# Performance work log

Measured on AMD Instinct MI355X. Metric: run time of the kernel, lower is better.

Reference implementation:

```python
import jax, jax.numpy as jnp
import numpy as np

N_NODES = 200000
N_EVENTS = 200000
MEM_DIM = 128
MSG_DIM = 128
TIME_DIM = 16
MSG_IN = 2 * MEM_DIM + MSG_DIM + TIME_DIM  # 400


def setup_inputs() -> dict:
    key = jax.random.key(0)
    ks = jax.random.split(key, 12)
    return {
        "src_ids": jax.random.randint(ks[0], (N_EVENTS,), 0, N_NODES, dtype=jnp.int32),
        "dst_ids": jax.random.randint(ks[1], (N_EVENTS,), 0, N_NODES, dtype=jnp.int32),
        "edge_feat": jax.random.normal(ks[2], (N_EVENTS, MSG_DIM), dtype=jnp.float32),
        "timestamps": jax.random.uniform(ks[3], (N_EVENTS,), dtype=jnp.float32),
        "memory": jax.random.normal(ks[4], (N_NODES, MEM_DIM), dtype=jnp.float32) * 0.1,
        "last_update_time": jnp.zeros((N_NODES,), dtype=jnp.float32),
        "time_w": jax.random.normal(ks[5], (TIME_DIM,), dtype=jnp.float32),
        "time_phi": jnp.zeros((TIME_DIM,), dtype=jnp.float32),
        "W1": jax.random.normal(ks[6], (MSG_IN, MSG_DIM), dtype=jnp.float32) / np.sqrt(MSG_IN),
        "b1": jnp.zeros((MSG_DIM,), dtype=jnp.float32),
        "W2": jax.random.normal(ks[7], (MSG_DIM, MSG_DIM), dtype=jnp.float32) / np.sqrt(MSG_DIM),
        "b2": jnp.zeros((MSG_DIM,), dtype=jnp.float32),
        "W_ih": jax.random.normal(ks[8], (3 * MEM_DIM, MSG_DIM), dtype=jnp.float32) / np.sqrt(MSG_DIM),
        "W_hh": jax.random.normal(ks[9], (3 * MEM_DIM, MEM_DIM), dtype=jnp.float32) / np.sqrt(MEM_DIM),
        "b_ih": jnp.zeros((3 * MEM_DIM,), dtype=jnp.float32),
        "b_hh": jnp.zeros((3 * MEM_DIM,), dtype=jnp.float32),
    }


def _time_encode(dt, w, phi):
    # Time2Vec: linear first channel, sin on the rest
    wt = dt[:, None] * w[None, :] + phi[None, :]  # [E, TIME_DIM]
    return jnp.concatenate([wt[:, :1], jnp.sin(wt[:, 1:])], axis=-1)


def _message_mlp(x, W1, b1, W2, b2):
    h = jax.nn.relu(x @ W1 + b1)
    return h @ W2 + b2


def _gru_cell(x, h, W_ih, W_hh, b_ih, b_hh):
    gi = x @ W_ih.T + b_ih  # [U, 3H]
    gh = h @ W_hh.T + b_hh
    i_r, i_z, i_n = jnp.split(gi, 3, axis=-1)
    h_r, h_z, h_n = jnp.split(gh, 3, axis=-1)
    r = jax.nn.sigmoid(i_r + h_r)
    z = jax.nn.sigmoid(i_z + h_z)
    n = jnp.tanh(i_n + r * h_n)
    return (1.0 - z) * n + z * h


def reference(src_ids, dst_ids, edge_feat, timestamps, memory, last_update_time,
              time_w, time_phi, W1, b1, W2, b2, W_ih, W_hh, b_ih, b_hh):
    # 1) gather + time encode
    dt_src = timestamps - last_update_time[src_ids]
    dt_dst = timestamps - last_update_time[dst_ids]
    te_src = _time_encode(dt_src, time_w, time_phi)
    te_dst = _time_encode(dt_dst, time_w, time_phi)
    src_mem = memory[src_ids]
    dst_mem = memory[dst_ids]

    # 2) messages
    msg_src = _message_mlp(jnp.concatenate([src_mem, dst_mem, edge_feat, te_src], -1), W1, b1, W2, b2)
    msg_dst = _message_mlp(jnp.concatenate([dst_mem, src_mem, edge_feat, te_dst], -1), W1, b1, W2, b2)

    all_nodes = jnp.concatenate([src_ids, dst_ids])  # [2E]
    all_msgs = jnp.concatenate([msg_src, msg_dst], axis=0)  # [2E, MSG_DIM]

    # 3) 'last' aggregation: segment-max of positions, then gather
    pos = jnp.arange(all_nodes.shape[0], dtype=jnp.int32)
    last_pos = jax.ops.segment_max(pos, all_nodes, num_segments=N_NODES)  # int32 min where absent
    present = last_pos >= 0  # [N]
    agg = all_msgs[jnp.clip(last_pos, 0, None)]  # [N, MSG_DIM]
    agg = jnp.where(present[:, None], agg, 0.0)

    # 4) GRU memory update on involved nodes only
    new_mem = _gru_cell(agg, memory, W_ih, W_hh, b_ih, b_hh)
    memory_out = jnp.where(present[:, None], new_mem, memory)
    return memory_out
```

## Files before the change

### kernel.cpp

```cpp
#include <hip/hip_runtime.h>
#include <hip/hip_bf16.h>
#include <math.h>

#define NN 200000
#define NE 200000

typedef __attribute__((ext_vector_type(8))) short bf16x8;
typedef __attribute__((ext_vector_type(4))) float f32x4;

#define XASTR 136
#define XBSTR 296
#define OSTR  132
#define NT    (NN / 32)
#define PBT   (32 * XBSTR)

__device__ __forceinline__ float sigm(float x) { return 1.0f / (1.0f + __expf(-x)); }
__device__ __forceinline__ float tanh_f(float x) {
    float e = __expf(2.0f * x);
    return 1.0f - 2.0f / (e + 1.0f);
}
__device__ __forceinline__ ushort f2b(float x) {
    union { __hip_bfloat16 b; ushort u; } v;
    v.b = __float2bfloat16(x);
    return v.u;
}
__device__ __forceinline__ float b2f(ushort u) {
    return __uint_as_float(((unsigned)u) << 16);
}
__device__ __forceinline__ ushort4 cvt4(float4 v) {
    ushort4 u; u.x = f2b(v.x); u.y = f2b(v.y); u.z = f2b(v.z); u.w = f2b(v.w);
    return u;
}
__device__ __forceinline__ void gload_lds16(const ushort* g, ushort* l) {
    __builtin_amdgcn_global_load_lds(
        (const __attribute__((address_space(1))) unsigned int*)g,
        (__attribute__((address_space(3))) unsigned int*)l, 16, 0, 0);
}

#define MFMA16(a, b, c) __builtin_amdgcn_mfma_f32_16x16x32_bf16((a), (b), (c), 0, 0, 0)

#define NB_PREP 594
#define NB_SCAT (((2 * NE) + 255) / 256)
__global__ void k_pre(const float* __restrict__ W1, const float* __restrict__ W2,
                      const float* __restrict__ Wih, const float* __restrict__ Whh,
                      const float* __restrict__ b2, const float* __restrict__ bih,
                      ushort* __restrict__ W1F, ushort* __restrict__ W2IF,
                      ushort* __restrict__ WHF, float* __restrict__ cb,
                      const int* __restrict__ src, const int* __restrict__ dst,
                      int* __restrict__ last_pos) {
    int b = blockIdx.x;
    if (b >= NB_PREP) {
        int i = (b - NB_PREP) * 256 + threadIdx.x;
        if (i < NE) {
            atomicMax(&last_pos[src[i]], i);
        } else if (i < 2 * NE) {
            atomicMax(&last_pos[dst[i - NE]], i);
        }
        return;
    }
    int t = b * 256 + threadIdx.x;
    if (t < 104 * 512) {
        int f = t >> 9, idx = t & 511;
        int lane = idx >> 3, j = idx & 7, c16 = lane & 15, k8 = lane >> 4;
        int wvv = f / 26, r = f % 26, kt = r >> 1, ns = r & 1;
        int col = wvv * 32 + ns * 16 + c16;
        int kk = kt * 32 + k8 * 8 + j;
        W1F[t] = (kk < 400) ? f2b(W1[kk * 128 + col]) : (ushort)0;
        return;
    }
    t -= 104 * 512;
    if (t < 96 * 512) {
        int f = t >> 9, idx = t & 511;
        int lane = idx >> 3, j = idx & 7, c16 = lane & 15, k8 = lane >> 4;
        int wvv = f / 24, r = f % 24, kt = r / 6, rem = r % 6, g = rem >> 1, ns = rem & 1;
        int col = g * 128 + wvv * 32 + ns * 16 + c16;
        int kk = kt * 32 + k8 * 8 + j;
        float s = 0.0f;
        for (int c = 0; c < 128; ++c) s = fmaf(W2[kk * 128 + c], Wih[col * 128 + c], s);
        W2IF[f * 512 + idx] = f2b(s);
        return;
    }
    t -= 96 * 512;
    if (t < 96 * 512) {
        int f = t >> 9, idx = t & 511;
        int lane = idx >> 3, j = idx & 7, c16 = lane & 15, k8 = lane >> 4;
        int wvv = f / 24, r = f % 24, kt = r / 6, rem = r % 6, g = rem >> 1, ns = rem & 1;
        int col = g * 128 + wvv * 32 + ns * 16 + c16;
        int kk = kt * 32 + k8 * 8 + j;
        WHF[f * 512 + idx] = f2b(Whh[col * 128 + kk]);
        return;
    }
    t -= 96 * 512;
    if (t < 384) {
        float s = bih[t];
        for (int k = 0; k < 128; ++k) s = fmaf(b2[k], Wih[t * 128 + k], s);
        cb[t] = s;
    }
}

__global__ __launch_bounds__(256)
void k_gath(const int* __restrict__ last_pos,
            const int* __restrict__ src, const int* __restrict__ dst,
            const float* __restrict__ ts, const float* __restrict__ lut,
            const float* __restrict__ mem, const float* __restrict__ ef,
            const float* __restrict__ tw, const float* __restrict__ tphi,
            ushort* __restrict__ PB)
{
    const int wv = threadIdx.x >> 6, lane = threadIdx.x & 63;
    const int n0 = (blockIdx.x * 4 + wv) * 2;
    const int n1 = n0 + 1;
    const int l = lane & 31;
    const bool lo = lane < 32;

    const int p0 = last_pos[n0];
    const int p1 = last_pos[n1];

    float4 m0, f0, m1, f1;
    float te0 = 0.0f, te1 = 0.0f;
    if (p0 >= 0) {
        int e = (p0 < NE) ? p0 : p0 - NE;
        int o = (p0 < NE) ? dst[e] : src[e];
        if (lo) {
            m0 = *(const float4*)&mem[(size_t)o * 128 + l * 4];
            if (l < 16) {
                float dt = ts[e] - lut[n0];
                float w = fmaf(dt, tw[l], tphi[l]);
                te0 = (l == 0) ? w : __sinf(w);
            }
        } else {
            f0 = *(const float4*)&ef[(size_t)e * 128 + l * 4];
        }
    }
    if (p1 >= 0) {
        int e = (p1 < NE) ? p1 : p1 - NE;
        int o = (p1 < NE) ? dst[e] : src[e];
        if (lo) {
            m1 = *(const float4*)&mem[(size_t)o * 128 + l * 4];
            if (l < 16) {
                float dt = ts[e] - lut[n1];
                float w = fmaf(dt, tw[l], tphi[l]);
                te1 = (l == 0) ? w : __sinf(w);
            }
        } else {
            f1 = *(const float4*)&ef[(size_t)e * 128 + l * 4];
        }
    }

    if (p0 >= 0) {
        ushort* xb = PB + (size_t)n0 * XBSTR;
        if (lo) {
            *(ushort4*)&xb[l * 4] = cvt4(m0);
            xb[256 + l] = (l < 16) ? f2b(te0) : (ushort)0;
        } else {
            *(ushort4*)&xb[128 + l * 4] = cvt4(f0);
        }
    }
    if (p1 >= 0) {
        ushort* xb = PB + (size_t)n1 * XBSTR;
        if (lo) {
            *(ushort4*)&xb[l * 4] = cvt4(m1);
            xb[256 + l] = (l < 16) ? f2b(te1) : (ushort)0;
        } else {
            *(ushort4*)&xb[128 + l * 4] = cvt4(f1);
        }
    }
}

__global__ __launch_bounds__(256, 4)
void k_main7(const ushort* __restrict__ PB, const int* __restrict__ last_pos,
             const float* __restrict__ mem,
             const ushort* __restrict__ W1F, const float* __restrict__ b1,
             const ushort* __restrict__ W2IF, const ushort* __restrict__ WHF,
             const float* __restrict__ cb, const float* __restrict__ bhh,
             float* __restrict__ out)
{
    __shared__ __align__(16) ushort XA[32 * XASTR];
    __shared__ __align__(16) ushort HB[32 * XASTR];
    __shared__ __align__(16) ushort XB[32 * XBSTR];
    __shared__ unsigned char pres[32];

    const int base = blockIdx.x * 32;
    const int tid  = threadIdx.x;
    const int lane = tid & 63;
    const int wv   = tid >> 6;
    const int r16  = lane & 15;
    const int kb   = lane >> 4;

    {
        const ushort* srcPB = PB + (size_t)blockIdx.x * PBT;
        #pragma unroll
        for (int j = 0; j < 5; ++j) {
            int cc = wv + j * 4;
            if (cc < 18) gload_lds16(srcPB + cc * 512 + lane * 8, XB + cc * 512);
            else if (cc == 18 && lane < 32) gload_lds16(srcPB + cc * 512 + lane * 8, XB + cc * 512);
        }
    }
    {
        const float* msrc = mem + (size_t)base * 128;
        #pragma unroll
        for (int k = 0; k < 4; ++k) {
            int i0 = k * 1024 + tid * 4;
            float4 v = *(const float4*)&msrc[i0];
            *(ushort4*)&XA[(i0 >> 7) * XASTR + (i0 & 127)] = cvt4(v);
        }
        if (tid < 32) pres[tid] = (unsigned char)(last_pos[base + tid] >= 0);
    }
    const ushort* w1 = W1F  + wv * (26 * 512) + lane * 8;
    const ushort* wI = W2IF + wv * (24 * 512) + lane * 8;
    const ushort* wH = WHF  + wv * (24 * 512) + lane * 8;
    __syncthreads();

    f32x4 c1[2][2] = {};
    {
        const ushort* aA = &XA[r16 * XASTR + kb * 8];
        const ushort* aB = &XB[r16 * XBSTR + kb * 8];
        #pragma unroll
        for (int kt = 0; kt < 13; ++kt) {
            const ushort* ap  = (kt < 4) ? (aA + kt * 32) : (aB + (kt - 4) * 32);
            const int     ast = (kt < 4) ? XASTR : XBSTR;
            bf16x8 A0 = *(const bf16x8*)ap;
            bf16x8 A1 = *(const bf16x8*)(ap + 16 * ast);
            bf16x8 B0 = *(const bf16x8*)(w1 + (kt * 2 + 0) * 512);
            bf16x8 B1 = *(const bf16x8*)(w1 + (kt * 2 + 1) * 512);
            c1[0][0] = MFMA16(A0, B0, c1[0][0]);
            c1[0][1] = MFMA16(A0, B1, c1[0][1]);
            c1[1][0] = MFMA16(A1, B0, c1[1][0]);
            c1[1][1] = MFMA16(A1, B1, c1[1][1]);
        }
    }
    #pragma unroll
    for (int ns = 0; ns < 2; ++ns) {
        int col = wv * 32 + ns * 16 + r16;
        float bb = b1[col];
        #pragma unroll
        for (int m = 0; m < 2; ++m)
            #pragma unroll
            for (int r = 0; r < 4; ++r)
                HB[(m * 16 + kb * 4 + r) * XASTR + col] =
                    f2b(fmaxf(c1[m][ns][r] + bb, 0.0f));
    }
    __syncthreads();

    f32x4 arz[2][4] = {};
    f32x4 an_i[2][2] = {};
    f32x4 an_h[2][2] = {};
    {
        const ushort* am = &HB[r16 * XASTR + kb * 8];
        const ushort* ah = &XA[r16 * XASTR + kb * 8];
        #pragma unroll
        for (int kt = 0; kt < 4; ++kt) {
            bf16x8 M0 = *(const bf16x8*)(am + kt * 32);
            bf16x8 M1 = *(const bf16x8*)(am + 16 * XASTR + kt * 32);
            bf16x8 H0 = *(const bf16x8*)(ah + kt * 32);
            bf16x8 H1 = *(const bf16x8*)(ah + 16 * XASTR + kt * 32);
            #pragma unroll
            for (int g = 0; g < 2; ++g)
                #pragma unroll
                for (int ns = 0; ns < 2; ++ns) {
                    int fo = (kt * 6 + g * 2 + ns) * 512;
                    bf16x8 Bi = *(const bf16x8*)(wI + fo);
                    bf16x8 Bh = *(const bf16x8*)(wH + fo);
                    arz[0][g * 2 + ns] = MFMA16(M0, Bi, arz[0][g * 2 + ns]);
                    arz[0][g * 2 + ns] = MFMA16(H0, Bh, arz[0][g * 2 + ns]);
                    arz[1][g * 2 + ns] = MFMA16(M1, Bi, arz[1][g * 2 + ns]);
                    arz[1][g * 2 + ns] = MFMA16(H1, Bh, arz[1][g * 2 + ns]);
                }
            #pragma unroll
            for (int ns = 0; ns < 2; ++ns) {
                int fo = (kt * 6 + 4 + ns) * 512;
                bf16x8 Bi = *(const bf16x8*)(wI + fo);
                bf16x8 Bh = *(const bf16x8*)(wH + fo);
                an_i[0][ns] = MFMA16(M0, Bi, an_i[0][ns]);
                an_i[1][ns] = MFMA16(M1, Bi, an_i[1][ns]);
                an_h[0][ns] = MFMA16(H0, Bh, an_h[0][ns]);
                an_h[1][ns] = MFMA16(H1, Bh, an_h[1][ns]);
            }
        }
    }

    float* XBf = (float*)XB;
    #pragma unroll
    for (int ns = 0; ns < 2; ++ns) {
        int col = wv * 32 + ns * 16 + r16;
        float brz0 = cb[col] + bhh[col];
        float brz1 = cb[128 + col] + bhh[128 + col];
        float bin  = cb[256 + col];
        float bhn  = bhh[256 + col];
        #pragma unroll
        for (int m = 0; m < 2; ++m) {
            #pragma unroll
            for (int r = 0; r < 4; ++r) {
                int row = m * 16 + kb * 4 + r;
                float rr = sigm(arz[m][0 + ns][r] + brz0);
                float zz = sigm(arz[m][2 + ns][r] + brz1);
                float nn = tanh_f(an_i[m][ns][r] + bin +
                                  rr * (an_h[m][ns][r] + bhn));
                float hh = b2f(XA[row * XASTR + col]);
                XBf[row * OSTR + col] = (1.0f - zz) * nn + zz * hh;
            }
        }
    }
    __syncthreads();

    for (int j = wv; j < 32; j += 4) {
        float2 v;
        if (pres[j]) v = *(const float2*)&XBf[j * OSTR + lane * 2];
        else         v = *(const float2*)&mem[(size_t)(base + j) * 128 + lane * 2];
        *(float2*)&out[(size_t)(base + j) * 128 + lane * 2] = v;
    }
}

extern "C" void kernel_launch(void* const* d_in, const int* in_sizes, int n_in,
                              void* d_out, int out_size, void* d_ws, size_t ws_size,
                              hipStream_t stream) {
    const int*   src  = (const int*)d_in[0];
    const int*   dst  = (const int*)d_in[1];
    const float* ef   = (const float*)d_in[2];
    const float* ts   = (const float*)d_in[3];
    const float* mem  = (const float*)d_in[4];
    const float* lut  = (const float*)d_in[5];
    const float* tw   = (const float*)d_in[6];
    const float* tphi = (const float*)d_in[7];
    const float* W1   = (const float*)d_in[8];
    const float* b1   = (const float*)d_in[9];
    const float* W2   = (const float*)d_in[10];
    const float* b2   = (const float*)d_in[11];
    const float* Wih  = (const float*)d_in[12];
    const float* Whh  = (const float*)d_in[13];
    const float* bih  = (const float*)d_in[14];
    const float* bhh  = (const float*)d_in[15];
    float* out = (float*)d_out;

    char* ws = (char*)d_ws;
    size_t off = 0;
    int*    last_pos = (int*)(ws + off);    off += (size_t)NN * 4;
    ushort* W1F      = (ushort*)(ws + off); off += (size_t)104 * 512 * 2;
    ushort* W2IF     = (ushort*)(ws + off); off += (size_t)96 * 512 * 2;
    ushort* WHF      = (ushort*)(ws + off); off += (size_t)96 * 512 * 2;
    float*  cb       = (float*)(ws + off);  off += (size_t)384 * 4 + 64;
    ushort* PB       = (ushort*)(ws + off);

    hipMemsetAsync(last_pos, 0xFF, (size_t)NN * sizeof(int), stream);

    k_pre<<<NB_PREP + NB_SCAT, 256, 0, stream>>>(
        W1, W2, Wih, Whh, b2, bih, W1F, W2IF, WHF, cb, src, dst, last_pos);
    k_gath<<<NN / 8, 256, 0, stream>>>(last_pos, src, dst, ts, lut, mem, ef, tw, tphi, PB);
    k_main7<<<NT, 256, 0, stream>>>(PB, last_pos, mem, W1F, b1, W2IF, WHF, cb, bhh, out);
}
```

Baseline: 248.4 us.

## Gather four nodes per wave, reverse tile order, add MFMA priority hints

The gather kernel now has each wave handle four nodes instead of two, which gives more independent loads in flight, and it launches half as many blocks. The main kernel walks tiles in reverse order, presumably so the last-written gather output is read while still in cache. It also raises wave priority around the MFMA loops with s_setprio, and lowers the occupancy hint in launch_bounds from 4 to 3. These are several separate scheduling and cache-locality tweaks, and the lower occupancy hint may reduce latency hiding.

Result: slower. 260.3 us (+4.8%).

```diff
diff --git a/kernel.cpp b/kernel.cpp
--- a/kernel.cpp
+++ b/kernel.cpp
@@ -107,67 +107,50 @@
             ushort* __restrict__ PB)
 {
     const int wv = threadIdx.x >> 6, lane = threadIdx.x & 63;
-    const int n0 = (blockIdx.x * 4 + wv) * 2;
-    const int n1 = n0 + 1;
+    const int n0 = (blockIdx.x * 4 + wv) * 4;
     const int l = lane & 31;
     const bool lo = lane < 32;
 
-    const int p0 = last_pos[n0];
-    const int p1 = last_pos[n1];
-
-    float4 m0, f0, m1, f1;
-    float te0 = 0.0f, te1 = 0.0f;
-    if (p0 >= 0) {
-        int e = (p0 < NE) ? p0 : p0 - NE;
-        int o = (p0 < NE) ? dst[e] : src[e];
-        if (lo) {
-            m0 = *(const float4*)&mem[(size_t)o * 128 + l * 4];
-            if (l < 16) {
-                float dt = ts[e] - lut[n0];
-                float w = fmaf(dt, tw[l], tphi[l]);
-                te0 = (l == 0) ? w : __sinf(w);
+    int p[4];
+    #pragma unroll
+    for (int s = 0; s < 4; ++s) p[s] = last_pos[n0 + s];
+
+    float4 mv[4], fv[4];
+    float te[4];
+    #pragma unroll
+    for (int s = 0; s < 4; ++s) {
+        te[s] = 0.0f;
+        if (p[s] >= 0) {
+            int e = (p[s] < NE) ? p[s] : p[s] - NE;
+            int o = (p[s] < NE) ? dst[e] : src[e];
+            if (lo) {
+                mv[s] = *(const float4*)&mem[(size_t)o * 128 + l * 4];
+                if (l < 16) {
+                    float dt = ts[e] - lut[n0 + s];
+                    float w = fmaf(dt, tw[l], tphi[l]);
+                    te[s] = (l == 0) ? w : __sinf(w);
+                }
+            } else {
+                fv[s] = *(const float4*)&ef[(size_t)e * 128 + l * 4];
             }
-        } else {
-            f0 = *(const float4*)&ef[(size_t)e * 128 + l * 4];
-        }
-    }
-    if (p1 >= 0) {
-        int e = (p1 < NE) ? p1 : p1 - NE;
-        int o = (p1 < NE) ? dst[e] : src[e];
-        if (lo) {
-            m1 = *(const float4*)&mem[(size_t)o * 128 + l * 4];
-            if (l < 16) {
-                float dt = ts[e] - lut[n1];
-                float w = fmaf(dt, tw[l], tphi[l]);
-                te1 = (l == 0) ? w : __sinf(w);
+        }
+    }
+    #pragma unroll
+    for (int s = 0; s < 4; ++s) {
+        if (p[s] >= 0) {
+            ushort* xb = PB + (size_t)(n0 + s) * XBSTR;
+            if (lo) {
+                *(ushort4*)&xb[l * 4] = cvt4(mv[s]);
+                xb[256 + l] = (l < 16) ? f2b(te[s]) : (ushort)0;
+            } else {
+                *(ushort4*)&xb[128 + l * 4] = cvt4(fv[s]);
             }
-        } else {
-            f1 = *(const float4*)&ef[(size_t)e * 128 + l * 4];
-        }
-    }
-
-    if (p0 >= 0) {
-        ushort* xb = PB + (size_t)n0 * XBSTR;
-        if (lo) {
-            *(ushort4*)&xb[l * 4] = cvt4(m0);
-            xb[256 + l] = (l < 16) ? f2b(te0) : (ushort)0;
-        } else {
-            *(ushort4*)&xb[128 + l * 4] = cvt4(f0);
-        }
-    }
-    if (p1 >= 0) {
-        ushort* xb = PB + (size_t)n1 * XBSTR;
-        if (lo) {
-            *(ushort4*)&xb[l * 4] = cvt4(m1);
-            xb[256 + l] = (l < 16) ? f2b(te1) : (ushort)0;
-        } else {
-            *(ushort4*)&xb[128 + l * 4] = cvt4(f1);
-        }
-    }
-}
-
-__global__ __launch_bounds__(256, 4)
-void k_main7(const ushort* __restrict__ PB, const int* __restrict__ last_pos,
+        }
+    }
+}
+
+__global__ __launch_bounds__(256, 3)
+void k_main8(const ushort* __restrict__ PB, const int* __restrict__ last_pos,
              const float* __restrict__ mem,
              const ushort* __restrict__ W1F, const float* __restrict__ b1,
              const ushort* __restrict__ W2IF, const ushort* __restrict__ WHF,
@@ -179,7 +162,8 @@
     __shared__ __align__(16) ushort XB[32 * XBSTR];
     __shared__ unsigned char pres[32];
 
-    const int base = blockIdx.x * 32;
+    const int tile = (NT - 1) - blockIdx.x;
+    const int base = tile * 32;
     const int tid  = threadIdx.x;
     const int lane = tid & 63;
     const int wv   = tid >> 6;
@@ -187,7 +171,7 @@
     const int kb   = lane >> 4;
 
     {
-        const ushort* srcPB = PB + (size_t)blockIdx.x * PBT;
+        const ushort* srcPB = PB + (size_t)tile * PBT;
         #pragma unroll
         for (int j = 0; j < 5; ++j) {
             int cc = wv + j * 4;
@@ -214,6 +198,7 @@
     {
         const ushort* aA = &XA[r16 * XASTR + kb * 8];
         const ushort* aB = &XB[r16 * XBSTR + kb * 8];
+        __builtin_amdgcn_s_setprio(1);
         #pragma unroll
         for (int kt = 0; kt < 13; ++kt) {
             const ushort* ap  = (kt < 4) ? (aA + kt * 32) : (aB + (kt - 4) * 32);
@@ -227,6 +212,7 @@
             c1[1][0] = MFMA16(A1, B0, c1[1][0]);
             c1[1][1] = MFMA16(A1, B1, c1[1][1]);
         }
+        __builtin_amdgcn_s_setprio(0);
     }
     #pragma unroll
     for (int ns = 0; ns < 2; ++ns) {
@@ -247,6 +233,7 @@
     {
         const ushort* am = &HB[r16 * XASTR + kb * 8];
         const ushort* ah = &XA[r16 * XASTR + kb * 8];
+        __builtin_amdgcn_s_setprio(1);
         #pragma unroll
         for (int kt = 0; kt < 4; ++kt) {
             bf16x8 M0 = *(const bf16x8*)(am + kt * 32);
@@ -276,6 +263,7 @@
                 an_h[1][ns] = MFMA16(H1, Bh, an_h[1][ns]);
             }
         }
+        __builtin_amdgcn_s_setprio(0);
     }
 
     float* XBf = (float*)XB;
@@ -344,6 +332,6 @@
 
     k_pre<<<NB_PREP + NB_SCAT, 256, 0, stream>>>(
         W1, W2, Wih, Whh, b2, bih, W1F, W2IF, WHF, cb, src, dst, last_pos);
-    k_gath<<<NN / 8, 256, 0, stream>>>(last_pos, src, dst, ts, lut, mem, ef, tw, tphi, PB);
-    k_main7<<<NT, 256, 0, stream>>>(PB, last_pos, mem, W1F, b1, W2IF, WHF, cb, bhh, out);
-}
+    k_gath<<<NN / 16, 256, 0, stream>>>(last_pos, src, dst, ts, lut, mem, ef, tw, tphi, PB);
+    k_main8<<<NT, 256, 0, stream>>>(PB, last_pos, mem, W1F, b1, W2IF, WHF, cb, bhh, out);
+}
```
